# Kernel optimization log

Measured on AMD Instinct MI355X. Metric: run time of the kernel, lower is better.

Reference implementation:

```python
import jax, jax.numpy as jnp
import numpy as np

B = 32768          # batch (replay-buffer minibatch)
OBS, ACT = 17, 6   # HalfCheetah-style dims
IN = OBS + ACT
H = 256            # hidden width hard-coded in the module
N = 10             # num_q_nets


def setup_inputs() -> dict:
    key = jax.random.key(0)
    ks = jax.random.split(key, 8)
    # PyTorch Linear default init: U(-1/sqrt(fan_in), 1/sqrt(fan_in)); scale randn similarly.
    s1, s2, s3 = 1.0 / np.sqrt(IN), 1.0 / np.sqrt(H), 1.0 / np.sqrt(H)
    return {
        "state": jax.random.normal(ks[0], (B, OBS), dtype=jnp.float32),
        "action": jax.random.uniform(ks[1], (B, ACT), dtype=jnp.float32, minval=-1.0, maxval=1.0),
        "W1": jax.random.normal(ks[2], (N, IN, H), dtype=jnp.float32) * s1,
        "b1": jax.random.normal(ks[3], (N, H), dtype=jnp.float32) * s1,
        "W2": jax.random.normal(ks[4], (N, H, H), dtype=jnp.float32) * s2,
        "b2": jax.random.normal(ks[5], (N, H), dtype=jnp.float32) * s2,
        "W3": jax.random.normal(ks[6], (N, H, 1), dtype=jnp.float32) * s3,
        "b3": jax.random.normal(ks[7], (N, 1), dtype=jnp.float32) * s3,
    }


def reference(state, action, W1, b1, W2, b2, W3, b3):
    # x: [B, OBS+ACT]
    x = jnp.concatenate([state, action], axis=1)
    # batched-over-ensemble GEMMs; n=ensemble member, b=batch
    h1 = jax.nn.relu(jnp.einsum("bi,nih->nbh", x, W1) + b1[:, None, :])   # [N,B,H]
    h2 = jax.nn.relu(jnp.einsum("nbh,nho->nbo", h1, W2) + b2[:, None, :])  # [N,B,H]
    out = jnp.einsum("nbh,nho->nbo", h2, W3) + b3[:, None, :]              # [N,B,1]
    return out
```

## Files before the change

kernel.cpp:

```cpp
#include <hip/hip_runtime.h>
#include <hip/hip_bf16.h>


typedef __attribute__((ext_vector_type(8))) short bf16x8;
typedef __attribute__((ext_vector_type(4))) float f32x4;
typedef __attribute__((ext_vector_type(2))) float f32x2;

#define B_TOTAL 32768
#define NQ 10
#define HDIM 256
#define BT 64

#define XP_ELEMS  (B_TOTAL * 32)
#define W1P_ELEMS (NQ * 16 * 64 * 8)
#define W2P_ELEMS (NQ * 8 * 16 * 64 * 8)

__device__ __forceinline__ unsigned short f2bf(float f) {
  unsigned int u = __float_as_uint(f);
  u = u + 0x7FFFu + ((u >> 16) & 1u);
  return (unsigned short)(u >> 16);
}

__device__ __forceinline__ unsigned int pk2bf(float a, float b) {
  union { __hip_bfloat162 h; unsigned int u; } cv;
  cv.h = __float22bfloat162_rn(make_float2(a, b));
  return cv.u;
}

__global__ void pack_all_kernel(const float* __restrict__ state,
                                const float* __restrict__ action,
                                const float* __restrict__ W1,
                                const float* __restrict__ b1,
                                const float* __restrict__ W2,
                                unsigned short* __restrict__ xp,
                                unsigned short* __restrict__ w1p,
                                unsigned short* __restrict__ w2p) {
  int t = blockIdx.x * 256 + threadIdx.x;
  const int NX  = B_TOTAL * 4;
  const int NW1 = NQ * 16 * 64;
  if (t < NX) {
    int b = t >> 2, seg = t & 3;
    unsigned short v[8];
    if (seg < 2) {
      const float* sp = state + (size_t)b * 17 + seg * 8;
#pragma unroll
      for (int j = 0; j < 8; j++) v[j] = f2bf(sp[j]);
    } else if (seg == 2) {
      v[0] = f2bf(state[(size_t)b * 17 + 16]);
#pragma unroll
      for (int j = 0; j < 6; j++) v[1 + j] = f2bf(action[(size_t)b * 6 + j]);
      v[7] = 0x3F80;
    } else {
#pragma unroll
      for (int j = 0; j < 8; j++) v[j] = 0;
    }
    *(uint4*)&xp[(size_t)t * 8] = *(const uint4*)v;
  } else if (t < NX + NW1) {
    int u = t - NX;
    int lane = u & 63, mt = (u >> 6) & 15, n = u >> 10;
    int m = lane & 15, q = lane >> 4;
    int outc = mt * 16 + m;
    unsigned short v[8];
#pragma unroll
    for (int j = 0; j < 8; j++) {
      int k = q * 8 + j;
      v[j] = (k < 23) ? f2bf(W1[(n * 23 + k) * 256 + outc])
           : (k == 23) ? f2bf(b1[n * 256 + outc]) : (unsigned short)0;
    }
    *(uint4*)&w1p[(size_t)u * 8] = *(const uint4*)v;
  } else {
    int u = t - NX - NW1;
    int lane = u & 63, mt = (u >> 6) & 15, kt = (u >> 10) & 7, n = u >> 13;
    int m = lane & 15, q = lane >> 4;
    int outc = mt * 16 + m;
    unsigned short v[8];
#pragma unroll
    for (int j = 0; j < 8; j++) {
      int h = kt * 32 + q * 8 + j;
      v[j] = f2bf(W2[((size_t)(n * 256 + h)) * 256 + outc]);
    }
    *(uint4*)&w2p[(size_t)u * 8] = *(const uint4*)v;
  }
}

__global__ __launch_bounds__(256, 4) void fused_ensemble_kernel(
    const unsigned short* __restrict__ xp,
    const unsigned short* __restrict__ w1p,
    const unsigned short* __restrict__ w2p,
    const float* __restrict__ b2,
    const float* __restrict__ W3,
    const float* __restrict__ b3,
    float* __restrict__ out) {
  __shared__ __align__(16) unsigned short hs[32 * BT * 8];
  __shared__ float red[4 * 64];

  const int tid = threadIdx.x;
  const int lane = tid & 63;
  const int w = tid >> 6;
  const int m = lane & 15;
  const int q = lane >> 4;

  const int n = blockIdx.x >> 9;
  const int row0 = (blockIdx.x & 511) * BT;

  f32x4 acc[4][4];

  {
    bf16x8 af1[4], bfr[4];
#pragma unroll
    for (int nt = 0; nt < 4; nt++) {
      int col = row0 + nt * 16 + m;
      bfr[nt] = *(const bf16x8*)(xp + (size_t)col * 32 + q * 8);
    }
#pragma unroll
    for (int mt = 0; mt < 4; mt++)
      af1[mt] = *(const bf16x8*)(w1p + (((size_t)n * 16 + w * 4 + mt) * 64 + lane) * 8);
#pragma unroll
    for (int mt = 0; mt < 4; mt++)
#pragma unroll
      for (int nt = 0; nt < 4; nt++) acc[mt][nt] = (f32x4)0.0f;
    __builtin_amdgcn_s_setprio(1);
#pragma unroll
    for (int nt = 0; nt < 4; nt++)
#pragma unroll
      for (int mt = 0; mt < 4; mt++)
        acc[mt][nt] = __builtin_amdgcn_mfma_f32_16x16x32_bf16(af1[mt], bfr[nt], acc[mt][nt], 0, 0, 0);
    __builtin_amdgcn_s_setprio(0);
  }

#pragma unroll
  for (int mt = 0; mt < 4; mt++) {
    int kq = w * 8 + mt * 2 + (q >> 1);
    int joff = (q & 1) * 4;
#pragma unroll
    for (int nt = 0; nt < 4; nt++) {
      int col = nt * 16 + m;
      f32x4 a = __builtin_elementwise_max(acc[mt][nt], (f32x4)0.0f);
      uint2 wv;
      wv.x = pk2bf(a.x, a.y);
      wv.y = pk2bf(a.z, a.w);
      *(uint2*)&hs[((size_t)kq * BT + col) * 8 + joff] = wv;
    }
  }

  const unsigned short* w2n = w2p + (size_t)n * (8 * 16 * 64 * 8);
  bf16x8 afb[2][4];
#pragma unroll
  for (int mt = 0; mt < 4; mt++)
    afb[0][mt] = *(const bf16x8*)(w2n + (((size_t)w * 4 + mt) * 64 + lane) * 8);
  f32x4 b2v[4];
#pragma unroll
  for (int mt = 0; mt < 4; mt++)
    b2v[mt] = *(const f32x4*)&b2[n * HDIM + (w * 4 + mt) * 16 + q * 4];
  __syncthreads();

  {
#pragma unroll
    for (int mt = 0; mt < 4; mt++)
#pragma unroll
      for (int nt = 0; nt < 4; nt++) acc[mt][nt] = b2v[mt];
#pragma unroll
    for (int kt = 0; kt < 8; kt++) {
      if (kt < 7) {
#pragma unroll
        for (int mt = 0; mt < 4; mt++)
          afb[(kt + 1) & 1][mt] =
              *(const bf16x8*)(w2n + (((size_t)(kt + 1) * 16 + w * 4 + mt) * 64 + lane) * 8);
      }
      bf16x8 bfr[4];
#pragma unroll
      for (int nt = 0; nt < 4; nt++)
        bfr[nt] = *(const bf16x8*)&hs[(((size_t)kt * 4 + q) * BT + nt * 16 + m) * 8];
      __builtin_amdgcn_s_setprio(1);
#pragma unroll
      for (int nt = 0; nt < 4; nt++)
#pragma unroll
        for (int mt = 0; mt < 4; mt++)
          acc[mt][nt] = __builtin_amdgcn_mfma_f32_16x16x32_bf16(afb[kt & 1][mt], bfr[nt],
                                                               acc[mt][nt], 0, 0, 0);
      __builtin_amdgcn_s_setprio(0);
    }
  }

  {
    f32x4 w3v[4];
#pragma unroll
    for (int mt = 0; mt < 4; mt++)
      w3v[mt] = *(const f32x4*)&W3[n * HDIM + (w * 4 + mt) * 16 + q * 4];
    float p[4];
#pragma unroll
    for (int nt = 0; nt < 4; nt++) {
      f32x2 s2 = (f32x2)0.0f;
#pragma unroll
      for (int mt = 0; mt < 4; mt++) {
        f32x4 a = __builtin_elementwise_max(acc[mt][nt], (f32x4)0.0f);
        s2 += a.lo * w3v[mt].lo;
        s2 += a.hi * w3v[mt].hi;
      }
      float s = s2.x + s2.y;
      s += __shfl_xor(s, 16, 64);
      s += __shfl_xor(s, 32, 64);
      p[nt] = s;
    }
    if (q == 0) {
#pragma unroll
      for (int nt = 0; nt < 4; nt++) red[w * 64 + nt * 16 + m] = p[nt];
    }
    __syncthreads();
    if (tid < BT) {
      float s = b3[n];
#pragma unroll
      for (int c = 0; c < 4; c++) s += red[c * 64 + tid];
      out[(size_t)n * B_TOTAL + row0 + tid] = s;
    }
  }
}

extern "C" void kernel_launch(void* const* d_in, const int* in_sizes, int n_in,
                              void* d_out, int out_size, void* d_ws, size_t ws_size,
                              hipStream_t stream) {
  const float* state  = (const float*)d_in[0];
  const float* action = (const float*)d_in[1];
  const float* W1 = (const float*)d_in[2];
  const float* b1 = (const float*)d_in[3];
  const float* W2 = (const float*)d_in[4];
  const float* b2 = (const float*)d_in[5];
  const float* W3 = (const float*)d_in[6];
  const float* b3 = (const float*)d_in[7];
  float* out = (float*)d_out;

  unsigned short* xp  = (unsigned short*)d_ws;
  unsigned short* w1p = (unsigned short*)((char*)d_ws + (size_t)XP_ELEMS * 2);
  unsigned short* w2p = (unsigned short*)((char*)d_ws + (size_t)(XP_ELEMS + W1P_ELEMS) * 2);

  pack_all_kernel<<<872, 256, 0, stream>>>(state, action, W1, b1, W2, xp, w1p, w2p);
  fused_ensemble_kernel<<<NQ * (B_TOTAL / BT), 256, 0, stream>>>(
      xp, w1p, w2p, b2, W3, b3, out);
}
```

Before: 118.3 us.

## Make ensemble kernel semi-persistent with XCD-aware tile mapping and input prefetch

Launches 1024 blocks, each processing 5 consecutive (net, batch-tile) tiles in a loop instead of one block per tile. Block indices are swizzled so that neighbouring tiles, which share weights, land on the same XCD, which should improve L2 reuse of W1/W2. The next tile's input fragment is prefetched while the current tile's output reduction runs, to hide global load latency. The cost is a serialized per-block loop, so latency inside each block is less hidden by parallel blocks, and there is less freedom to balance load across CUs.

```diff
diff --git a/kernel.cpp b/kernel.cpp
--- a/kernel.cpp
+++ b/kernel.cpp
@@ -100,118 +100,135 @@
   const int m = lane & 15;
   const int q = lane >> 4;
 
-  const int n = blockIdx.x >> 9;
-  const int row0 = (blockIdx.x & 511) * BT;
+  const int bid = blockIdx.x;
+  const int tile0 = ((bid & 7) * 128 + (bid >> 3)) * 5;
 
   f32x4 acc[4][4];
+  bf16x8 bfr[4];
 
   {
-    bf16x8 af1[4], bfr[4];
-#pragma unroll
-    for (int nt = 0; nt < 4; nt++) {
-      int col = row0 + nt * 16 + m;
-      bfr[nt] = *(const bf16x8*)(xp + (size_t)col * 32 + q * 8);
-    }
+    int row0 = (tile0 & 511) * BT;
+#pragma unroll
+    for (int nt = 0; nt < 4; nt++)
+      bfr[nt] = *(const bf16x8*)(xp + (size_t)(row0 + nt * 16 + m) * 32 + q * 8);
+  }
+
+#pragma unroll 1
+  for (int tt = 0; tt < 5; ++tt) {
+    const int t = tile0 + tt;
+    const int n = t >> 9;
+    const int row0 = (t & 511) * BT;
+
+    {
+      bf16x8 af1[4];
+#pragma unroll
+      for (int mt = 0; mt < 4; mt++)
+        af1[mt] = *(const bf16x8*)(w1p + (((size_t)n * 16 + w * 4 + mt) * 64 + lane) * 8);
+#pragma unroll
+      for (int mt = 0; mt < 4; mt++)
+#pragma unroll
+        for (int nt = 0; nt < 4; nt++) acc[mt][nt] = (f32x4)0.0f;
+      __builtin_amdgcn_s_setprio(1);
+#pragma unroll
+      for (int nt = 0; nt < 4; nt++)
+#pragma unroll
+        for (int mt = 0; mt < 4; mt++)
+          acc[mt][nt] = __builtin_amdgcn_mfma_f32_16x16x32_bf16(af1[mt], bfr[nt], acc[mt][nt], 0, 0, 0);
+      __builtin_amdgcn_s_setprio(0);
+    }
+
+#pragma unroll
+    for (int mt = 0; mt < 4; mt++) {
+      int kq = w * 8 + mt * 2 + (q >> 1);
+      int joff = (q & 1) * 4;
+#pragma unroll
+      for (int nt = 0; nt < 4; nt++) {
+        int col = nt * 16 + m;
+        f32x4 a = __builtin_elementwise_max(acc[mt][nt], (f32x4)0.0f);
+        uint2 wv;
+        wv.x = pk2bf(a.x, a.y);
+        wv.y = pk2bf(a.z, a.w);
+        *(uint2*)&hs[((size_t)kq * BT + col) * 8 + joff] = wv;
+      }
+    }
+
+    const unsigned short* w2n = w2p + (size_t)n * (8 * 16 * 64 * 8);
+    bf16x8 afb[2][4];
 #pragma unroll
     for (int mt = 0; mt < 4; mt++)
-      af1[mt] = *(const bf16x8*)(w1p + (((size_t)n * 16 + w * 4 + mt) * 64 + lane) * 8);
+      afb[0][mt] = *(const bf16x8*)(w2n + (((size_t)w * 4 + mt) * 64 + lane) * 8);
+    f32x4 b2v[4];
 #pragma unroll
     for (int mt = 0; mt < 4; mt++)
-#pragma unroll
-      for (int nt = 0; nt < 4; nt++) acc[mt][nt] = (f32x4)0.0f;
-    __builtin_amdgcn_s_setprio(1);
-#pragma unroll
-    for (int nt = 0; nt < 4; nt++)
-#pragma unroll
-      for (int mt = 0; mt < 4; mt++)
-        acc[mt][nt] = __builtin_amdgcn_mfma_f32_16x16x32_bf16(af1[mt], bfr[nt], acc[mt][nt], 0, 0, 0);
-    __builtin_amdgcn_s_setprio(0);
-  }
-
-#pragma unroll
-  for (int mt = 0; mt < 4; mt++) {
-    int kq = w * 8 + mt * 2 + (q >> 1);
-    int joff = (q & 1) * 4;
-#pragma unroll
-    for (int nt = 0; nt < 4; nt++) {
-      int col = nt * 16 + m;
-      f32x4 a = __builtin_elementwise_max(acc[mt][nt], (f32x4)0.0f);
-      uint2 wv;
-      wv.x = pk2bf(a.x, a.y);
-      wv.y = pk2bf(a.z, a.w);
-      *(uint2*)&hs[((size_t)kq * BT + col) * 8 + joff] = wv;
-    }
-  }
-
-  const unsigned short* w2n = w2p + (size_t)n * (8 * 16 * 64 * 8);
-  bf16x8 afb[2][4];
-#pragma unroll
-  for (int mt = 0; mt < 4; mt++)
-    afb[0][mt] = *(const bf16x8*)(w2n + (((size_t)w * 4 + mt) * 64 + lane) * 8);
-  f32x4 b2v[4];
-#pragma unroll
-  for (int mt = 0; mt < 4; mt++)
-    b2v[mt] = *(const f32x4*)&b2[n * HDIM + (w * 4 + mt) * 16 + q * 4];
-  __syncthreads();
-
-  {
-#pragma unroll
-    for (int mt = 0; mt < 4; mt++)
-#pragma unroll
-      for (int nt = 0; nt < 4; nt++) acc[mt][nt] = b2v[mt];
-#pragma unroll
-    for (int kt = 0; kt < 8; kt++) {
-      if (kt < 7) {
-#pragma unroll
-        for (int mt = 0; mt < 4; mt++)
-          afb[(kt + 1) & 1][mt] =
-              *(const bf16x8*)(w2n + (((size_t)(kt + 1) * 16 + w * 4 + mt) * 64 + lane) * 8);
-      }
-      bf16x8 bfr[4];
+      b2v[mt] = *(const f32x4*)&b2[n * HDIM + (w * 4 + mt) * 16 + q * 4];
+    __syncthreads();
+
+    {
+#pragma unroll
+      for (int mt = 0; mt < 4; mt++)
+#pragma unroll
+        for (int nt = 0; nt < 4; nt++) acc[mt][nt] = b2v[mt];
+#pragma unroll
+      for (int kt = 0; kt < 8; kt++) {
+        if (kt < 7) {
+#pragma unroll
+          for (int mt = 0; mt < 4; mt++)
+            afb[(kt + 1) & 1][mt] =
+                *(const bf16x8*)(w2n + (((size_t)(kt + 1) * 16 + w * 4 + mt) * 64 + lane) * 8);
+        }
+        bf16x8 bq[4];
+#pragma unroll
+        for (int nt = 0; nt < 4; nt++)
+          bq[nt] = *(const bf16x8*)&hs[(((size_t)kt * 4 + q) * BT + nt * 16 + m) * 8];
+        __builtin_amdgcn_s_setprio(1);
+#pragma unroll
+        for (int nt = 0; nt < 4; nt++)
+#pragma unroll
+          for (int mt = 0; mt < 4; mt++)
+            acc[mt][nt] = __builtin_amdgcn_mfma_f32_16x16x32_bf16(afb[kt & 1][mt], bq[nt],
+                                                                 acc[mt][nt], 0, 0, 0);
+        __builtin_amdgcn_s_setprio(0);
+      }
+    }
+
+    if (tt < 4) {
+      int row0n = ((t + 1) & 511) * BT;
 #pragma unroll
       for (int nt = 0; nt < 4; nt++)
-        bfr[nt] = *(const bf16x8*)&hs[(((size_t)kt * 4 + q) * BT + nt * 16 + m) * 8];
-      __builtin_amdgcn_s_setprio(1);
-#pragma unroll
-      for (int nt = 0; nt < 4; nt++)
-#pragma unroll
-        for (int mt = 0; mt < 4; mt++)
-          acc[mt][nt] = __builtin_amdgcn_mfma_f32_16x16x32_bf16(afb[kt & 1][mt], bfr[nt],
-                                                               acc[mt][nt], 0, 0, 0);
-      __builtin_amdgcn_s_setprio(0);
-    }
-  }
-
-  {
-    f32x4 w3v[4];
-#pragma unroll
-    for (int mt = 0; mt < 4; mt++)
-      w3v[mt] = *(const f32x4*)&W3[n * HDIM + (w * 4 + mt) * 16 + q * 4];
-    float p[4];
-#pragma unroll
-    for (int nt = 0; nt < 4; nt++) {
-      f32x2 s2 = (f32x2)0.0f;
-#pragma unroll
-      for (int mt = 0; mt < 4; mt++) {
-        f32x4 a = __builtin_elementwise_max(acc[mt][nt], (f32x4)0.0f);
-        s2 += a.lo * w3v[mt].lo;
-        s2 += a.hi * w3v[mt].hi;
-      }
-      float s = s2.x + s2.y;
-      s += __shfl_xor(s, 16, 64);
-      s += __shfl_xor(s, 32, 64);
-      p[nt] = s;
-    }
-    if (q == 0) {
-#pragma unroll
-      for (int nt = 0; nt < 4; nt++) red[w * 64 + nt * 16 + m] = p[nt];
-    }
-    __syncthreads();
-    if (tid < BT) {
-      float s = b3[n];
-#pragma unroll
-      for (int c = 0; c < 4; c++) s += red[c * 64 + tid];
-      out[(size_t)n * B_TOTAL + row0 + tid] = s;
+        bfr[nt] = *(const bf16x8*)(xp + (size_t)(row0n + nt * 16 + m) * 32 + q * 8);
+    }
+
+    {
+      f32x4 w3v[4];
+#pragma unroll
+      for (int mt = 0; mt < 4; mt++)
+        w3v[mt] = *(const f32x4*)&W3[n * HDIM + (w * 4 + mt) * 16 + q * 4];
+      float p[4];
+#pragma unroll
+      for (int nt = 0; nt < 4; nt++) {
+        f32x2 s2 = (f32x2)0.0f;
+#pragma unroll
+        for (int mt = 0; mt < 4; mt++) {
+          f32x4 a = __builtin_elementwise_max(acc[mt][nt], (f32x4)0.0f);
+          s2 += a.lo * w3v[mt].lo;
+          s2 += a.hi * w3v[mt].hi;
+        }
+        float s = s2.x + s2.y;
+        s += __shfl_xor(s, 16, 64);
+        s += __shfl_xor(s, 32, 64);
+        p[nt] = s;
+      }
+      if (q == 0) {
+#pragma unroll
+        for (int nt = 0; nt < 4; nt++) red[w * 64 + nt * 16 + m] = p[nt];
+      }
+      __syncthreads();
+      if (tid < BT) {
+        float s = b3[n];
+#pragma unroll
+        for (int c = 0; c < 4; c++) s += red[c * 64 + tid];
+        out[(size_t)n * B_TOTAL + row0 + tid] = s;
+      }
     }
   }
 }
@@ -234,6 +251,6 @@
   unsigned short* w2p = (unsigned short*)((char*)d_ws + (size_t)(XP_ELEMS + W1P_ELEMS) * 2);
 
   pack_all_kernel<<<872, 256, 0, stream>>>(state, action, W1, b1, W2, xp, w1p, w2p);
-  fused_ensemble_kernel<<<NQ * (B_TOTAL / BT), 256, 0, stream>>>(
+  fused_ensemble_kernel<<<1024, 256, 0, stream>>>(
       xp, w1p, w2p, b2, W3, b3, out);
 }
```

Result: slower. 176.6 us (+49.2%).
